# Kernel optimization log

Hardware: AMD Instinct MI355X
Metric: run time of the kernel (lower is better)

## Reference

```python
import jax, jax.numpy as jnp
import numpy as np

N, E, D, L = 50000, 800000, 64, 3
EPS = 1e-5


def setup_inputs() -> dict:
    key = jax.random.key(0)
    ks = jax.random.split(key, 12)
    x = jax.random.normal(ks[0], (N, D), dtype=jnp.float32)
    edge_index = jax.random.randint(ks[1], (2, E), 0, N, dtype=jnp.int64)
    w = lambda k: jax.random.normal(k, (L, D, D), dtype=jnp.float32) * 0.1
    return {
        "x": x,
        "edge_index": edge_index,
        "Wq": w(ks[2]), "bq": jnp.zeros((L, D), jnp.float32),
        "Wk": w(ks[3]), "bk": jnp.zeros((L, D), jnp.float32),
        "Wv": w(ks[4]), "bv": jnp.zeros((L, D), jnp.float32),
        "Ws": w(ks[5]), "bs": jnp.zeros((L, D), jnp.float32),
        "gamma": jnp.ones((L - 1, D), jnp.float32),
        "beta": jnp.zeros((L - 1, D), jnp.float32),
    }


def _transformer_conv(x, src, dst, Wq, bq, Wk, bk, Wv, bv, Ws, bs):
    # PyG TransformerConv, heads=1, concat=True, root_weight=True, beta=False
    n = x.shape[0]
    d = x.shape[1]
    q = x @ Wq + bq          # [N, D] query of target nodes
    k = x @ Wk + bk          # [N, D] key of source nodes
    v = x @ Wv + bv          # [N, D] value of source nodes
    skip = x @ Ws + bs       # root/skip term on target nodes
    scale = 1.0 / jnp.sqrt(jnp.asarray(d, x.dtype))
    s = jnp.sum(q[dst] * k[src], axis=-1) * scale        # [E] edge scores
    # segment softmax over incoming edges of each destination node
    m = jax.ops.segment_max(s, dst, num_segments=n)       # [N]
    e = jnp.exp(s - m[dst])                               # [E]
    denom = jax.ops.segment_sum(e, dst, num_segments=n)   # [N]
    alpha = e / denom[dst]                                # [E]
    agg = jax.ops.segment_sum(alpha[:, None] * v[src], dst, num_segments=n)  # [N, D]
    return agg + skip


def _batch_norm(x, gamma, beta):
    # nn.BatchNorm1d training-mode forward: batch stats over node dim, biased var
    mean = jnp.mean(x, axis=0)
    var = jnp.mean((x - mean) ** 2, axis=0)
    return gamma * (x - mean) * jax.lax.rsqrt(var + EPS) + beta


def reference(x, edge_index, Wq, bq, Wk, bk, Wv, bv, Ws, bs, gamma, beta):
    src, dst = edge_index[0], edge_index[1]
    num_layers = Wq.shape[0]
    h = x
    for l in range(num_layers):
        h = _transformer_conv(h, src, dst, Wq[l], bq[l], Wk[l], bk[l],
                              Wv[l], bv[l], Ws[l], bs[l])
        if l != num_layers - 1:
            h = _batch_norm(h, gamma[l], beta[l])
            h = jax.nn.relu(h)
    return h
```

## Files before the change

kernel.cpp:

```cpp
#include <hip/hip_runtime.h>
#include <math.h>

#define N_NODES 50000
#define N_EDGES 800000
#define EPSV 1e-5f
#define PROJ_NT 16
#define SCAN_NB ((N_NODES + 255) / 256)

__device__ __forceinline__ unsigned short f2bf(float f) {
    unsigned u = __float_as_uint(f);
    unsigned r = (u + 0x7fffu + ((u >> 16) & 1u)) >> 16;
    return (unsigned short)r;
}
__device__ __forceinline__ float bflo(unsigned u) { return __uint_as_float(u << 16); }
__device__ __forceinline__ float bfhi(unsigned u) { return __uint_as_float(u & 0xffff0000u); }


__global__ __launch_bounds__(256) void count_kernel(const int* __restrict__ dst,
                                                    int* __restrict__ cnt) {
    int e = blockIdx.x * 256 + threadIdx.x;
    if (e < N_EDGES) atomicAdd(&cnt[dst[e]], 1);
}

__global__ __launch_bounds__(256) void scan_blocksum(const int* __restrict__ cnt,
                                                     int* __restrict__ bsum) {
    __shared__ int red[256];
    int t = threadIdx.x;
    int i = blockIdx.x * 256 + t;
    red[t] = (i < N_NODES) ? cnt[i] : 0;
    __syncthreads();
#pragma unroll
    for (int o = 128; o > 0; o >>= 1) {
        if (t < o) red[t] += red[t + o];
        __syncthreads();
    }
    if (t == 0) bsum[blockIdx.x] = red[0];
}

__global__ __launch_bounds__(256) void scan_bsum(int* __restrict__ bsum) {
    __shared__ int buf[256];
    int t = threadIdx.x;
    int v = (t < SCAN_NB) ? bsum[t] : 0;
    buf[t] = v;
    __syncthreads();
#pragma unroll
    for (int o = 1; o < 256; o <<= 1) {
        int tv = (t >= o) ? buf[t - o] : 0;
        __syncthreads();
        buf[t] += tv;
        __syncthreads();
    }
    if (t < SCAN_NB) bsum[t] = buf[t] - v;
}

__global__ __launch_bounds__(256) void scan_final(int* __restrict__ cnt_cursor,
                                                  const int* __restrict__ bsum,
                                                  int* __restrict__ row_off) {
    __shared__ int buf[256];
    int t = threadIdx.x;
    int i = blockIdx.x * 256 + t;
    int v = (i < N_NODES) ? cnt_cursor[i] : 0;
    buf[t] = v;
    __syncthreads();
#pragma unroll
    for (int o = 1; o < 256; o <<= 1) {
        int tv = (t >= o) ? buf[t - o] : 0;
        __syncthreads();
        buf[t] += tv;
        __syncthreads();
    }
    int excl = buf[t] - v + bsum[blockIdx.x];
    if (i < N_NODES) {
        row_off[i]    = excl;
        cnt_cursor[i] = excl;
    }
    if (i == N_NODES) row_off[N_NODES] = N_EDGES;
}

__global__ __launch_bounds__(256) void scatter_kernel(const int* __restrict__ src,
                                                      const int* __restrict__ dst,
                                                      int* __restrict__ cursor,
                                                      unsigned short* __restrict__ ssrc) {
    int e = blockIdx.x * 256 + threadIdx.x;
    if (e < N_EDGES) {
        int d = dst[e];
        int p = atomicAdd(&cursor[d], 1);
        ssrc[p] = (unsigned short)src[e];
    }
}

__global__ __launch_bounds__(256) void fill_dst_kernel(const int* __restrict__ row_off,
                                                       unsigned short* __restrict__ sdst) {
    int n = blockIdx.x * 256 + threadIdx.x;
    if (n >= N_NODES) return;
    int b = row_off[n], e2 = row_off[n + 1];
    for (int p = b; p < e2; ++p) sdst[p] = (unsigned short)n;
}

template<bool BN>
__global__ __launch_bounds__(256) void proj_kernel(
    const float* __restrict__ hin,
    const float* __restrict__ Wq, const float* __restrict__ Wk,
    const float* __restrict__ Wv, const float* __restrict__ Ws,
    const float* __restrict__ bq, const float* __restrict__ bk,
    const float* __restrict__ bv, const float* __restrict__ bs,
    const float* __restrict__ bnp, const float* __restrict__ gamma,
    const float* __restrict__ beta,
    float* __restrict__ qb, unsigned short* __restrict__ kb,
    unsigned short* __restrict__ vb, float* __restrict__ skb)
{
    __shared__ float xs[16][64];
    const int t = threadIdx.x;
    const int m = t >> 6, c = t & 63;
    const float* Wm = (m == 0) ? Wq : (m == 1) ? Wk : (m == 2) ? Wv : Ws;
    const float* bm = (m == 0) ? bq : (m == 1) ? bk : (m == 2) ? bv : bs;
    float*          obase_f = ((m == 0) ? qb : skb) + c;
    unsigned short* obase_h = ((m == 1) ? kb : vb) + c;

    float w[64];
#pragma unroll
    for (int i = 0; i < 64; i++) w[i] = Wm[i * 64 + c];
    const float bias = bm[c];

    const int jj = t >> 4, i0 = (t & 15) * 4;
    float4 mu4, rs4, ga4, be4;
    if (BN) {
        mu4 = *(const float4*)&bnp[i0];
        rs4 = *(const float4*)&bnp[64 + i0];
        ga4 = *(const float4*)&gamma[i0];
        be4 = *(const float4*)&beta[i0];
    }

    const int nbase = blockIdx.x * PROJ_NT;
    for (int tile = 0; tile < PROJ_NT / 16; ++tile) {
        const int n0 = nbase + tile * 16;
        __syncthreads();
        {
            int node = n0 + jj;
            float4 xv = make_float4(0.f, 0.f, 0.f, 0.f);
            if (node < N_NODES) xv = *(const float4*)&hin[node * 64 + i0];
            if (BN) {
                xv.x = fmaxf(fmaf(ga4.x * (xv.x - mu4.x), rs4.x, be4.x), 0.f);
                xv.y = fmaxf(fmaf(ga4.y * (xv.y - mu4.y), rs4.y, be4.y), 0.f);
                xv.z = fmaxf(fmaf(ga4.z * (xv.z - mu4.z), rs4.z, be4.z), 0.f);
                xv.w = fmaxf(fmaf(ga4.w * (xv.w - mu4.w), rs4.w, be4.w), 0.f);
            }
            *(float4*)&xs[jj][i0] = xv;
        }
        __syncthreads();
#pragma unroll 4
        for (int j = 0; j < 16; j++) {
            const int node = n0 + j;
            if (node >= N_NODES) break;
            float a0 = bias, a1 = 0.f, a2 = 0.f, a3 = 0.f;
#pragma unroll
            for (int i4 = 0; i4 < 16; i4++) {
                float4 xv = *(const float4*)&xs[j][i4 * 4];
                a0 = fmaf(xv.x, w[i4 * 4 + 0], a0);
                a1 = fmaf(xv.y, w[i4 * 4 + 1], a1);
                a2 = fmaf(xv.z, w[i4 * 4 + 2], a2);
                a3 = fmaf(xv.w, w[i4 * 4 + 3], a3);
            }
            float r = (a0 + a1) + (a2 + a3);
            if (m == 0 || m == 3) obase_f[(size_t)node * 64] = r;
            else                  obase_h[(size_t)node * 64] = f2bf(r);
        }
    }
}

__global__ __launch_bounds__(256) void edge_kernel(const float* __restrict__ qb,
                                                   const unsigned short* __restrict__ kb,
                                                   const unsigned short* __restrict__ ssrc,
                                                   const unsigned short* __restrict__ sdst,
                                                   float* __restrict__ s_out) {
    int idx = blockIdx.x * 256 + threadIdx.x;
    int e   = idx >> 3;
    int l8  = idx & 7;
    if (e >= N_EDGES) return;
    int s = ssrc[e], d = sdst[e];
    const float4* qp = (const float4*)&qb[(size_t)d * 64 + l8 * 8];
    float4 q0 = qp[0], q1 = qp[1];
    uint4 kw = *(const uint4*)&kb[(size_t)s * 64 + l8 * 8];
    float acc = q0.x * bflo(kw.x) + q0.y * bfhi(kw.x)
              + q0.z * bflo(kw.y) + q0.w * bfhi(kw.y)
              + q1.x * bflo(kw.z) + q1.y * bfhi(kw.z)
              + q1.z * bflo(kw.w) + q1.w * bfhi(kw.w);
    acc += __shfl_xor(acc, 1);
    acc += __shfl_xor(acc, 2);
    acc += __shfl_xor(acc, 4);
    if (l8 == 0) s_out[e] = acc * 0.125f;
}

__global__ __launch_bounds__(256) void agg_kernel(const float* __restrict__ s_arr,
                                                  const unsigned short* __restrict__ vb,
                                                  const unsigned short* __restrict__ ssrc,
                                                  const int* __restrict__ row_off,
                                                  const float* __restrict__ skb,
                                                  float* __restrict__ out) {
    int tid  = blockIdx.x * 256 + threadIdx.x;
    int lane = threadIdx.x & 63;
    int l8   = lane & 7;
    int g    = (tid >> 6) * 8 + (lane >> 3);
    bool valid = g < N_NODES;
    int beg = 0, end = 0;
    float4 sk0 = make_float4(0, 0, 0, 0), sk1 = sk0;
    if (valid) {
        beg = row_off[g];
        end = row_off[g + 1];
        const float4* skp = (const float4*)&skb[(size_t)g * 64 + l8 * 8];
        sk0 = skp[0];
        sk1 = skp[1];
    }

    float mx = -INFINITY;
    for (int p = beg + l8; p < end; p += 8) mx = fmaxf(mx, s_arr[p]);
    mx = fmaxf(mx, __shfl_xor(mx, 1));
    mx = fmaxf(mx, __shfl_xor(mx, 2));
    mx = fmaxf(mx, __shfl_xor(mx, 4));

    const uint4* vw = (const uint4*)vb;
    const int sbase = lane & 56;
    float lsum = 0.f;
    float a0 = 0, a1 = 0, a2 = 0, a3 = 0, a4 = 0, a5 = 0, a6 = 0, a7 = 0;
    int base = beg;
    while (true) {
        int cnt = end - base;
        cnt = cnt < 0 ? 0 : (cnt > 8 ? 8 : cnt);
        int c = max(cnt, __shfl_xor(cnt, 8));
        c = max(c, __shfl_xor(c, 16));
        int cntm = max(c, __shfl_xor(c, 32));
        if (cntm == 0) break;
        float my_e = 0.f;
        int   my_s = 0;
        if (l8 < cnt) {
            my_e = __expf(s_arr[base + l8] - mx);
            my_s = (int)ssrc[base + l8];
        }
        lsum += my_e;
#pragma unroll 2
        for (int j = 0; j < cntm; ++j) {
            float w  = __shfl(my_e, sbase + j);
            int   sv = __shfl(my_s, sbase + j);
            uint4 vv = vw[(size_t)sv * 8 + l8];
            a0 = fmaf(w, bflo(vv.x), a0); a1 = fmaf(w, bfhi(vv.x), a1);
            a2 = fmaf(w, bflo(vv.y), a2); a3 = fmaf(w, bfhi(vv.y), a3);
            a4 = fmaf(w, bflo(vv.z), a4); a5 = fmaf(w, bfhi(vv.z), a5);
            a6 = fmaf(w, bflo(vv.w), a6); a7 = fmaf(w, bfhi(vv.w), a7);
        }
        base += 8;
    }
    lsum += __shfl_xor(lsum, 1);
    lsum += __shfl_xor(lsum, 2);
    lsum += __shfl_xor(lsum, 4);
    if (valid) {
        float inv = (end > beg) ? 1.f / lsum : 0.f;
        float4 r0, r1;
        r0.x = fmaf(a0, inv, sk0.x); r0.y = fmaf(a1, inv, sk0.y);
        r0.z = fmaf(a2, inv, sk0.z); r0.w = fmaf(a3, inv, sk0.w);
        r1.x = fmaf(a4, inv, sk1.x); r1.y = fmaf(a5, inv, sk1.y);
        r1.z = fmaf(a6, inv, sk1.z); r1.w = fmaf(a7, inv, sk1.w);
        float4* op = (float4*)&out[(size_t)g * 64 + l8 * 8];
        op[0] = r0;
        op[1] = r1;
    }
}

__global__ __launch_bounds__(256) void bn_stats_kernel(const float* __restrict__ h,
                                                       float* __restrict__ partials) {
    __shared__ float red[256], red2[256];
    int t = threadIdx.x;
    int d = t & 63, part = t >> 6;
    float s = 0.f, s2 = 0.f;
    for (int r = blockIdx.x * 4 + part; r < N_NODES; r += gridDim.x * 4) {
        float v = h[r * 64 + d];
        s += v;
        s2 = fmaf(v, v, s2);
    }
    red[t] = s; red2[t] = s2;
    __syncthreads();
    if (t < 64) {
        s  = red[t] + red[t + 64] + red[t + 128] + red[t + 192];
        s2 = red2[t] + red2[t + 64] + red2[t + 128] + red2[t + 192];
        partials[blockIdx.x * 128 + t]      = s;
        partials[blockIdx.x * 128 + 64 + t] = s2;
    }
}

__global__ void bn_final_kernel(const float* __restrict__ partials,
                                float* __restrict__ bnp) {
    __shared__ float sh[128];
    int t = threadIdx.x;
    float a = 0.f;
    for (int b = 0; b < 256; ++b) a += partials[b * 128 + t];
    sh[t] = a;
    __syncthreads();
    if (t < 64) {
        float mean = sh[t] * (1.0f / N_NODES);
        float var  = sh[64 + t] * (1.0f / N_NODES) - mean * mean;
        bnp[t]      = mean;
        bnp[64 + t] = rsqrtf(var + EPSV);
    }
}


extern "C" void kernel_launch(void* const* d_in, const int* in_sizes, int n_in,
                              void* d_out, int out_size, void* d_ws, size_t ws_size,
                              hipStream_t stream) {
    const float* x     = (const float*)d_in[0];
    const int*   ei    = (const int*)d_in[1];
    const float* Wq    = (const float*)d_in[2];
    const float* bq    = (const float*)d_in[3];
    const float* Wk    = (const float*)d_in[4];
    const float* bk    = (const float*)d_in[5];
    const float* Wv    = (const float*)d_in[6];
    const float* bv    = (const float*)d_in[7];
    const float* Ws    = (const float*)d_in[8];
    const float* bs    = (const float*)d_in[9];
    const float* gamma = (const float*)d_in[10];
    const float* beta  = (const float*)d_in[11];
    float* out = (float*)d_out;

    char* wsp = (char*)d_ws;
    size_t off = 0;
    auto alloc = [&](size_t bytes) -> void* {
        void* p = wsp + off;
        off += (bytes + 255) / 256 * 256;
        return p;
    };
    float*          qb       = (float*)alloc((size_t)N_NODES * 64 * 4);
    unsigned short* kb       = (unsigned short*)alloc((size_t)N_NODES * 64 * 2);
    unsigned short* vb       = (unsigned short*)alloc((size_t)N_NODES * 64 * 2);
    float*          skb      = (float*)alloc((size_t)N_NODES * 64 * 4);
    float*          hbuf     = (float*)alloc((size_t)N_NODES * 64 * 4);
    float*          s_arr    = (float*)alloc((size_t)N_EDGES * 4);
    int*            row_off  = (int*)alloc((size_t)(N_NODES + 1) * 4);
    int*            cursor   = (int*)alloc((size_t)N_NODES * 4);
    unsigned short* ssrc     = (unsigned short*)alloc((size_t)N_EDGES * 2);
    unsigned short* sdst     = (unsigned short*)alloc((size_t)N_EDGES * 2);
    int*            bsum     = (int*)alloc((size_t)SCAN_NB * 4);
    float*          partials = (float*)alloc(256 * 128 * 4);
    float*          bnp      = (float*)alloc(128 * 4);

    const int* src = ei;
    const int* dst = ei + N_EDGES;

    hipMemsetAsync(cursor, 0, N_NODES * 4, stream);
    count_kernel<<<(N_EDGES + 255) / 256, 256, 0, stream>>>(dst, cursor);
    scan_blocksum<<<SCAN_NB, 256, 0, stream>>>(cursor, bsum);
    scan_bsum<<<1, 256, 0, stream>>>(bsum);
    scan_final<<<SCAN_NB, 256, 0, stream>>>(cursor, bsum, row_off);
    scatter_kernel<<<(N_EDGES + 255) / 256, 256, 0, stream>>>(src, dst, cursor, ssrc);
    fill_dst_kernel<<<SCAN_NB, 256, 0, stream>>>(row_off, sdst);

    const int proj_grid = (N_NODES + PROJ_NT - 1) / PROJ_NT;
    const int edge_grid = (N_EDGES * 8 + 255) / 256;
    const int agg_grid  = (N_NODES + 31) / 32;

    for (int l = 0; l < 3; l++) {
        const float* hin = (l == 0) ? x : hbuf;
        if (l == 0) {
            proj_kernel<false><<<proj_grid, 256, 0, stream>>>(
                hin, Wq, Wk, Wv, Ws, bq, bk, bv, bs,
                bnp, gamma, beta, qb, kb, vb, skb);
        } else {
            proj_kernel<true><<<proj_grid, 256, 0, stream>>>(
                hin, Wq + l * 4096, Wk + l * 4096, Wv + l * 4096, Ws + l * 4096,
                bq + l * 64, bk + l * 64, bv + l * 64, bs + l * 64,
                bnp, gamma + (l - 1) * 64, beta + (l - 1) * 64, qb, kb, vb, skb);
        }
        edge_kernel<<<edge_grid, 256, 0, stream>>>(qb, kb, ssrc, sdst, s_arr);
        float* o = (l == 2) ? out : hbuf;
        agg_kernel<<<agg_grid, 256, 0, stream>>>(s_arr, vb, ssrc, row_off, skb, o);
        if (l < 2) {
            bn_stats_kernel<<<256, 256, 0, stream>>>(hbuf, partials);
            bn_final_kernel<<<1, 128, 0, stream>>>(partials, bnp);
        }
    }
}
```

Measured before the change: 358.3 us.

## Fuse BatchNorm statistics into aggregation epilogue via shared and global atomics

The aggregation kernel now accumulates per-feature sum and sum of squares of its outputs into shared memory with atomics, then adds them to a global 128-float buffer. This replaces the separate stats kernel that re-read the full hidden buffer, and the final kernel reads the sums directly and resets them for the next layer. The scatter store of sorted source indices is also made nontemporal. In exchange it adds heavy shared-atomic contention on 128 addresses per block, about 1563 global atomic adds per address, and order-dependent float summation.

```diff
diff --git a/kernel.cpp b/kernel.cpp
--- a/kernel.cpp
+++ b/kernel.cpp
@@ -37,9 +37,11 @@
     if (t == 0) bsum[blockIdx.x] = red[0];
 }
 
-__global__ __launch_bounds__(256) void scan_bsum(int* __restrict__ bsum) {
+__global__ __launch_bounds__(256) void scan_bsum(int* __restrict__ bsum,
+                                                 float* __restrict__ sums) {
     __shared__ int buf[256];
     int t = threadIdx.x;
+    if (t < 128) sums[t] = 0.f;
     int v = (t < SCAN_NB) ? bsum[t] : 0;
     buf[t] = v;
     __syncthreads();
@@ -85,7 +87,7 @@
     if (e < N_EDGES) {
         int d = dst[e];
         int p = atomicAdd(&cursor[d], 1);
-        ssrc[p] = (unsigned short)src[e];
+        __builtin_nontemporal_store((unsigned short)src[e], &ssrc[p]);
     }
 }
 
@@ -191,12 +193,19 @@
     if (l8 == 0) s_out[e] = acc * 0.125f;
 }
 
+template<bool STATS>
 __global__ __launch_bounds__(256) void agg_kernel(const float* __restrict__ s_arr,
                                                   const unsigned short* __restrict__ vb,
                                                   const unsigned short* __restrict__ ssrc,
                                                   const int* __restrict__ row_off,
                                                   const float* __restrict__ skb,
-                                                  float* __restrict__ out) {
+                                                  float* __restrict__ out,
+                                                  float* __restrict__ sums) {
+    __shared__ float sm[128];
+    if (STATS) {
+        if (threadIdx.x < 128) sm[threadIdx.x] = 0.f;
+        __syncthreads();
+    }
     int tid  = blockIdx.x * 256 + threadIdx.x;
     int lane = threadIdx.x & 63;
     int l8   = lane & 7;
@@ -252,54 +261,47 @@
     lsum += __shfl_xor(lsum, 1);
     lsum += __shfl_xor(lsum, 2);
     lsum += __shfl_xor(lsum, 4);
+    float inv = (end > beg) ? 1.f / lsum : 0.f;
+    float4 r0, r1;
+    r0.x = fmaf(a0, inv, sk0.x); r0.y = fmaf(a1, inv, sk0.y);
+    r0.z = fmaf(a2, inv, sk0.z); r0.w = fmaf(a3, inv, sk0.w);
+    r1.x = fmaf(a4, inv, sk1.x); r1.y = fmaf(a5, inv, sk1.y);
+    r1.z = fmaf(a6, inv, sk1.z); r1.w = fmaf(a7, inv, sk1.w);
     if (valid) {
-        float inv = (end > beg) ? 1.f / lsum : 0.f;
-        float4 r0, r1;
-        r0.x = fmaf(a0, inv, sk0.x); r0.y = fmaf(a1, inv, sk0.y);
-        r0.z = fmaf(a2, inv, sk0.z); r0.w = fmaf(a3, inv, sk0.w);
-        r1.x = fmaf(a4, inv, sk1.x); r1.y = fmaf(a5, inv, sk1.y);
-        r1.z = fmaf(a6, inv, sk1.z); r1.w = fmaf(a7, inv, sk1.w);
         float4* op = (float4*)&out[(size_t)g * 64 + l8 * 8];
         op[0] = r0;
         op[1] = r1;
     }
-}
-
-__global__ __launch_bounds__(256) void bn_stats_kernel(const float* __restrict__ h,
-                                                       float* __restrict__ partials) {
-    __shared__ float red[256], red2[256];
+    if (STATS) {
+        if (valid) {
+            int d0 = l8 * 8;
+            atomicAdd(&sm[d0 + 0], r0.x); atomicAdd(&sm[64 + d0 + 0], r0.x * r0.x);
+            atomicAdd(&sm[d0 + 1], r0.y); atomicAdd(&sm[64 + d0 + 1], r0.y * r0.y);
+            atomicAdd(&sm[d0 + 2], r0.z); atomicAdd(&sm[64 + d0 + 2], r0.z * r0.z);
+            atomicAdd(&sm[d0 + 3], r0.w); atomicAdd(&sm[64 + d0 + 3], r0.w * r0.w);
+            atomicAdd(&sm[d0 + 4], r1.x); atomicAdd(&sm[64 + d0 + 4], r1.x * r1.x);
+            atomicAdd(&sm[d0 + 5], r1.y); atomicAdd(&sm[64 + d0 + 5], r1.y * r1.y);
+            atomicAdd(&sm[d0 + 6], r1.z); atomicAdd(&sm[64 + d0 + 6], r1.z * r1.z);
+            atomicAdd(&sm[d0 + 7], r1.w); atomicAdd(&sm[64 + d0 + 7], r1.w * r1.w);
+        }
+        __syncthreads();
+        if (threadIdx.x < 128) atomicAdd(&sums[threadIdx.x], sm[threadIdx.x]);
+    }
+}
+
+__global__ void bn_final_kernel(float* __restrict__ sums, float* __restrict__ bnp) {
     int t = threadIdx.x;
-    int d = t & 63, part = t >> 6;
-    float s = 0.f, s2 = 0.f;
-    for (int r = blockIdx.x * 4 + part; r < N_NODES; r += gridDim.x * 4) {
-        float v = h[r * 64 + d];
-        s += v;
-        s2 = fmaf(v, v, s2);
-    }
-    red[t] = s; red2[t] = s2;
+    float mean = 0.f, var = 0.f;
+    if (t < 64) {
+        mean = sums[t] * (1.0f / N_NODES);
+        var  = sums[64 + t] * (1.0f / N_NODES) - mean * mean;
+    }
     __syncthreads();
     if (t < 64) {
-        s  = red[t] + red[t + 64] + red[t + 128] + red[t + 192];
-        s2 = red2[t] + red2[t + 64] + red2[t + 128] + red2[t + 192];
-        partials[blockIdx.x * 128 + t]      = s;
-        partials[blockIdx.x * 128 + 64 + t] = s2;
-    }
-}
-
-__global__ void bn_final_kernel(const float* __restrict__ partials,
-                                float* __restrict__ bnp) {
-    __shared__ float sh[128];
-    int t = threadIdx.x;
-    float a = 0.f;
-    for (int b = 0; b < 256; ++b) a += partials[b * 128 + t];
-    sh[t] = a;
-    __syncthreads();
-    if (t < 64) {
-        float mean = sh[t] * (1.0f / N_NODES);
-        float var  = sh[64 + t] * (1.0f / N_NODES) - mean * mean;
         bnp[t]      = mean;
         bnp[64 + t] = rsqrtf(var + EPSV);
     }
+    sums[t] = 0.f;
 }
 
 
@@ -327,19 +329,19 @@
         off += (bytes + 255) / 256 * 256;
         return p;
     };
-    float*          qb       = (float*)alloc((size_t)N_NODES * 64 * 4);
-    unsigned short* kb       = (unsigned short*)alloc((size_t)N_NODES * 64 * 2);
-    unsigned short* vb       = (unsigned short*)alloc((size_t)N_NODES * 64 * 2);
-    float*          skb      = (float*)alloc((size_t)N_NODES * 64 * 4);
-    float*          hbuf     = (float*)alloc((size_t)N_NODES * 64 * 4);
-    float*          s_arr    = (float*)alloc((size_t)N_EDGES * 4);
-    int*            row_off  = (int*)alloc((size_t)(N_NODES + 1) * 4);
-    int*            cursor   = (int*)alloc((size_t)N_NODES * 4);
-    unsigned short* ssrc     = (unsigned short*)alloc((size_t)N_EDGES * 2);
-    unsigned short* sdst     = (unsigned short*)alloc((size_t)N_EDGES * 2);
-    int*            bsum     = (int*)alloc((size_t)SCAN_NB * 4);
-    float*          partials = (float*)alloc(256 * 128 * 4);
-    float*          bnp      = (float*)alloc(128 * 4);
+    float*          qb      = (float*)alloc((size_t)N_NODES * 64 * 4);
+    unsigned short* kb      = (unsigned short*)alloc((size_t)N_NODES * 64 * 2);
+    unsigned short* vb      = (unsigned short*)alloc((size_t)N_NODES * 64 * 2);
+    float*          skb     = (float*)alloc((size_t)N_NODES * 64 * 4);
+    float*          hbuf    = (float*)alloc((size_t)N_NODES * 64 * 4);
+    float*          s_arr   = (float*)alloc((size_t)N_EDGES * 4);
+    int*            row_off = (int*)alloc((size_t)(N_NODES + 1) * 4);
+    int*            cursor  = (int*)alloc((size_t)N_NODES * 4);
+    unsigned short* ssrc    = (unsigned short*)alloc((size_t)N_EDGES * 2);
+    unsigned short* sdst    = (unsigned short*)alloc((size_t)N_EDGES * 2);
+    int*            bsum    = (int*)alloc((size_t)SCAN_NB * 4);
+    float*          sums    = (float*)alloc(128 * 4);
+    float*          bnp     = (float*)alloc(128 * 4);
 
     const int* src = ei;
     const int* dst = ei + N_EDGES;
@@ -347,7 +349,7 @@
     hipMemsetAsync(cursor, 0, N_NODES * 4, stream);
     count_kernel<<<(N_EDGES + 255) / 256, 256, 0, stream>>>(dst, cursor);
     scan_blocksum<<<SCAN_NB, 256, 0, stream>>>(cursor, bsum);
-    scan_bsum<<<1, 256, 0, stream>>>(bsum);
+    scan_bsum<<<1, 256, 0, stream>>>(bsum, sums);
     scan_final<<<SCAN_NB, 256, 0, stream>>>(cursor, bsum, row_off);
     scatter_kernel<<<(N_EDGES + 255) / 256, 256, 0, stream>>>(src, dst, cursor, ssrc);
     fill_dst_kernel<<<SCAN_NB, 256, 0, stream>>>(row_off, sdst);
@@ -370,10 +372,13 @@
         }
         edge_kernel<<<edge_grid, 256, 0, stream>>>(qb, kb, ssrc, sdst, s_arr);
         float* o = (l == 2) ? out : hbuf;
-        agg_kernel<<<agg_grid, 256, 0, stream>>>(s_arr, vb, ssrc, row_off, skb, o);
         if (l < 2) {
-            bn_stats_kernel<<<256, 256, 0, stream>>>(hbuf, partials);
-            bn_final_kernel<<<1, 128, 0, stream>>>(partials, bnp);
-        }
-    }
-}
+            agg_kernel<true><<<agg_grid, 256, 0, stream>>>(s_arr, vb, ssrc, row_off,
+                                                           skb, o, sums);
+            bn_final_kernel<<<1, 128, 0, stream>>>(sums, bnp);
+        } else {
+            agg_kernel<false><<<agg_grid, 256, 0, stream>>>(s_arr, vb, ssrc, row_off,
+                                                            skb, o, sums);
+        }
+    }
+}
```

Result: slower. 430.2 us (+20.1%).
